# Kernel tuning notes

Measured on AMD Instinct MI355X. Metric: run time of the kernel, lower is better.

The kernel has to match this reference:

```python
import jax, jax.numpy as jnp
import numpy as np

N = 100000      # nodes
E = 1600000     # graph edges
P = 100000      # pos/neg candidate edges
D_IN = 128
D_H = 128
ALPHA = 0.1
NUM_LAYERS = 3


def _linear_params(key, d_in, d_out):
    k1, k2 = jax.random.split(key)
    s = 1.0 / np.sqrt(d_in)
    W = jax.random.uniform(k1, (d_in, d_out), minval=-s, maxval=s, dtype=jnp.float32)
    b = jax.random.uniform(k2, (d_out,), minval=-s, maxval=s, dtype=jnp.float32)
    return W, b


def setup_inputs() -> dict:
    key = jax.random.key(0)
    ks = jax.random.split(key, 12)
    x = jax.random.normal(ks[0], (N, D_IN), dtype=jnp.float32)
    src = jax.random.randint(ks[1], (E,), 0, N)
    dst = jax.random.randint(ks[2], (E,), 0, N)
    pos_src = jax.random.randint(ks[3], (P,), 0, N)
    pos_dst = jax.random.randint(ks[4], (P,), 0, N)
    neg_src = jax.random.randint(ks[5], (P,), 0, N)
    neg_dst = jax.random.randint(ks[6], (P,), 0, N)
    lin1_w, lin1_b = _linear_params(ks[7], D_IN, D_H)
    lin2_w, lin2_b = _linear_params(ks[8], D_H, D_H)
    p1_w, p1_b = _linear_params(ks[9], D_H, D_H)
    p2_w, p2_b = _linear_params(ks[10], D_H, D_H)
    p3_w, p3_b = _linear_params(ks[11], D_H, 1)
    # GPR gamma coefficients: alpha*(1-alpha)^k, last = (1-alpha)^L
    gamma = ALPHA * (1.0 - ALPHA) ** np.arange(NUM_LAYERS + 1, dtype=np.float32)
    gamma[-1] = (1.0 - ALPHA) ** NUM_LAYERS
    gamma = jnp.asarray(gamma, dtype=jnp.float32)
    return {
        "x": x, "lin1_w": lin1_w, "lin1_b": lin1_b, "lin2_w": lin2_w, "lin2_b": lin2_b,
        "gamma": gamma, "p1_w": p1_w, "p1_b": p1_b, "p2_w": p2_w, "p2_b": p2_b,
        "p3_w": p3_w, "p3_b": p3_b,
        "src": src, "dst": dst,
        "pos_src": pos_src, "pos_dst": pos_dst, "neg_src": neg_src, "neg_dst": neg_dst,
    }


def _graph_conv(h, src, dst, n):
    # DGL GraphConv(weight=False, bias=False), norm='both':
    # out = D_in^{-1/2} A (D_out^{-1/2} h), degrees clamped to >= 1
    ones = jnp.ones(src.shape[0], dtype=h.dtype)
    deg_out = jnp.clip(jax.ops.segment_sum(ones, src, num_segments=n), 1.0)
    deg_in = jnp.clip(jax.ops.segment_sum(ones, dst, num_segments=n), 1.0)
    h = h * jax.lax.rsqrt(deg_out)[:, None]
    agg = jax.ops.segment_sum(h[src], dst, num_segments=n)  # [N, D]
    return agg * jax.lax.rsqrt(deg_in)[:, None]


def _predictor(e, p1_w, p1_b, p2_w, p2_b, p3_w, p3_b):
    e = jax.nn.relu(e @ p1_w + p1_b)
    e = jax.nn.relu(e @ p2_w + p2_b)
    return e @ p3_w + p3_b  # [P, 1]


def reference(x, lin1_w, lin1_b, lin2_w, lin2_b, gamma, p1_w, p1_b, p2_w, p2_b,
              p3_w, p3_b, src, dst, pos_src, pos_dst, neg_src, neg_dst):
    n = x.shape[0]
    h = jax.nn.relu(x @ lin1_w + lin1_b)
    h = h @ lin2_w + lin2_b
    rep = gamma[0] * h
    for l in range(NUM_LAYERS):
        h = _graph_conv(h, src, dst, n)
        rep = rep + gamma[l + 1] * h  # full-graph blocks: dstnodes == all nodes
    h = rep
    h_pos = _predictor(h[pos_src] * h[pos_dst], p1_w, p1_b, p2_w, p2_b, p3_w, p3_b)
    h_neg = _predictor(h[neg_src] * h[neg_dst], p1_w, p1_b, p2_w, p2_b, p3_w, p3_b)
    return (h_pos, h_neg)
```

## Files before the change

### kernel.cpp

```cpp
#include <hip/hip_runtime.h>

#define D 128
#define HBINS 16384
#define HCHUNKS 32

typedef _Float16 half8 __attribute__((ext_vector_type(8)));
typedef float floatx4 __attribute__((ext_vector_type(4)));

__host__ __device__ static inline int cdiv(int a, int b){ return (a + b - 1) / b; }

__global__ __launch_bounds__(256) void hist_kernel(const int* __restrict__ vals, int E,
                                                   int* __restrict__ part)
{
    __shared__ int h[HBINS];
    const int r = blockIdx.x / HCHUNKS;
    const int c = blockIdx.x % HCHUNKS;
    for (int i = threadIdx.x; i < HBINS; i += 256) h[i] = 0;
    __syncthreads();

    int elen = cdiv(E, HCHUNKS);
    elen = (elen + 3) & ~3;
    const int lo = c * elen;
    const int hi = min(E, lo + elen);
    if (lo < hi) {
        const int nfull = (hi - lo) >> 2;
        const int4* v4 = (const int4*)(vals + lo);
        for (int i = threadIdx.x; i < nfull; i += 256) {
            const int4 v = v4[i];
            if ((v.x >> 14) == r) atomicAdd(&h[v.x & (HBINS - 1)], 1);
            if ((v.y >> 14) == r) atomicAdd(&h[v.y & (HBINS - 1)], 1);
            if ((v.z >> 14) == r) atomicAdd(&h[v.z & (HBINS - 1)], 1);
            if ((v.w >> 14) == r) atomicAdd(&h[v.w & (HBINS - 1)], 1);
        }
        for (int i = lo + (nfull << 2) + threadIdx.x; i < hi; i += 256) {
            const int v = vals[i];
            if ((v >> 14) == r) atomicAdd(&h[v & (HBINS - 1)], 1);
        }
    }
    __syncthreads();
    int* dstp = part + (size_t)blockIdx.x * HBINS;
    for (int i = threadIdx.x; i < HBINS; i += 256) dstp[i] = h[i];
}

__global__ __launch_bounds__(256) void hist_reduce(const int* __restrict__ partA,
                                                   const int* __restrict__ partB,
                                                   int* __restrict__ cnt_in,
                                                   float* __restrict__ dinv_out,
                                                   float* __restrict__ dinv_in, int n)
{
    const int i = blockIdx.x * 256 + threadIdx.x;
    if (i >= n) return;
    const int r = i >> 14, b = i & (HBINS - 1);
    const size_t base = ((size_t)r * HCHUNKS) * HBINS + b;
    int so = 0, si = 0;
    #pragma unroll
    for (int c = 0; c < HCHUNKS; ++c) {
        so += partA[base + (size_t)c * HBINS];
        si += partB[base + (size_t)c * HBINS];
    }
    dinv_out[i] = rsqrtf(fmaxf((float)so, 1.0f));
    dinv_in[i]  = rsqrtf(fmaxf((float)si, 1.0f));
    cnt_in[i] = si;
}


__global__ __launch_bounds__(256) void scan_partial(const int* __restrict__ cnt,
                                                    int* __restrict__ pre,
                                                    int* __restrict__ blk_sums, int n)
{
    __shared__ int lds[256];
    int t = threadIdx.x;
    int base = blockIdx.x * 1024 + t * 4;
    int v0 = 0, v1 = 0, v2 = 0, v3 = 0;
    if (base + 0 < n) v0 = cnt[base + 0];
    if (base + 1 < n) v1 = cnt[base + 1];
    if (base + 2 < n) v2 = cnt[base + 2];
    if (base + 3 < n) v3 = cnt[base + 3];
    int ts = v0 + v1 + v2 + v3;
    lds[t] = ts;
    __syncthreads();
    for (int off = 1; off < 256; off <<= 1) {
        int add = (t >= off) ? lds[t - off] : 0;
        __syncthreads();
        lds[t] += add;
        __syncthreads();
    }
    int excl = lds[t] - ts;
    if (base + 0 < n) pre[base + 0] = excl;
    if (base + 1 < n) pre[base + 1] = excl + v0;
    if (base + 2 < n) pre[base + 2] = excl + v0 + v1;
    if (base + 3 < n) pre[base + 3] = excl + v0 + v1 + v2;
    if (t == 255) blk_sums[blockIdx.x] = lds[255];
}

__global__ void scan_blk(const int* __restrict__ blk_sums, int* __restrict__ blk_off, int nblk)
{
    if (threadIdx.x == 0 && blockIdx.x == 0) {
        int run = 0;
        for (int j = 0; j < nblk; ++j) { blk_off[j] = run; run += blk_sums[j]; }
    }
}

__global__ __launch_bounds__(256) void scan_final(const int* __restrict__ pre,
                                                  const int* __restrict__ blk_off,
                                                  int* __restrict__ row_start,
                                                  int* __restrict__ fill_ptr, int n, int E)
{
    int i = blockIdx.x * 256 + threadIdx.x;
    if (i < n) {
        int v = pre[i] + blk_off[i >> 10];
        row_start[i] = v;
        fill_ptr[i]  = v;
    }
    if (i == 0) row_start[n] = E;
}

__global__ __launch_bounds__(256) void fill_kernel(const int* __restrict__ src,
                                                   const int* __restrict__ dst,
                                                   int* __restrict__ fill_ptr,
                                                   int* __restrict__ esrc, int E)
{
    int i = blockIdx.x * 256 + threadIdx.x;
    if (i < E) {
        int p = atomicAdd(&fill_ptr[dst[i]], 1);
        esrc[p] = src[i];
    }
}

__global__ __launch_bounds__(256) void wt_kernel(const float* __restrict__ W,
                                                 _Float16* __restrict__ Wt)
{
    __shared__ float tile[32][33];
    const int b = blockIdx.x;
    const int tx = b & 3, ty = b >> 2;
    const int t = threadIdx.x;
    const int r = t >> 3, c4 = (t & 7) * 4;
    const float4 v = *(const float4*)&W[(size_t)(ty * 32 + r) * D + tx * 32 + c4];
    tile[r][c4 + 0] = v.x; tile[r][c4 + 1] = v.y;
    tile[r][c4 + 2] = v.z; tile[r][c4 + 3] = v.w;
    __syncthreads();
    _Float16* dst = Wt + (size_t)(tx * 32 + r) * D + ty * 32 + c4;
    dst[0] = (_Float16)tile[c4 + 0][r];
    dst[1] = (_Float16)tile[c4 + 1][r];
    dst[2] = (_Float16)tile[c4 + 2][r];
    dst[3] = (_Float16)tile[c4 + 3][r];
}

__global__ __launch_bounds__(256, 4) void conv_f16(const _Float16* __restrict__ hin,
                                                   _Float16* __restrict__ hout,
                                                   float* __restrict__ rep,
                                                   const int* __restrict__ row_start,
                                                   const int* __restrict__ esrc,
                                                   const float* __restrict__ dinv_out,
                                                   const float* __restrict__ dinv_in,
                                                   const float* __restrict__ gamma,
                                                   int lidx, int n)
{
    const int node = (blockIdx.x * 256 + threadIdx.x) >> 4;
    const int sub  = threadIdx.x & 15;
    if (node >= n) return;
    const int rs = row_start[node];
    const int re = row_start[node + 1];
    const half8* hb = (const half8*)hin;

    float acc[8] = {0.f, 0.f, 0.f, 0.f, 0.f, 0.f, 0.f, 0.f};
    int i = rs;
    for (; i + 1 < re; i += 2) {
        const int s0 = esrc[i];
        const int s1 = esrc[i + 1];
        const float c0 = dinv_out[s0];
        const float c1 = dinv_out[s1];
        const half8 v0 = hb[(size_t)s0 * 16 + sub];
        const half8 v1 = hb[(size_t)s1 * 16 + sub];
        #pragma unroll
        for (int j = 0; j < 8; ++j)
            acc[j] += (float)v0[j] * c0 + (float)v1[j] * c1;
    }
    if (i < re) {
        const int s0 = esrc[i];
        const float c0 = dinv_out[s0];
        const half8 v0 = hb[(size_t)s0 * 16 + sub];
        #pragma unroll
        for (int j = 0; j < 8; ++j)
            acc[j] += (float)v0[j] * c0;
    }

    const float di = dinv_in[node];
    const float g  = gamma[lidx];
    half8 o;
    #pragma unroll
    for (int j = 0; j < 8; ++j) {
        acc[j] *= di;
        o[j] = (_Float16)acc[j];
    }
    ((half8*)hout)[(size_t)node * 16 + sub] = o;

    floatx4* rp = (floatx4*)(rep + (size_t)node * D + sub * 8);
    floatx4 r0 = rp[0], r1 = rp[1];
    r0[0] += g * acc[0]; r0[1] += g * acc[1]; r0[2] += g * acc[2]; r0[3] += g * acc[3];
    r1[0] += g * acc[4]; r1[1] += g * acc[5]; r1[2] += g * acc[6]; r1[3] += g * acc[7];
    rp[0] = r0; rp[1] = r1;
}

__device__ __forceinline__ int lds_off(int r, int chunk)
{
    return r * D + ((chunk ^ (r & 15)) << 3);
}

template<int MODE>
__global__ __launch_bounds__(256, 2) void gemm_mfma(const float* __restrict__ Xf,
                                                    const _Float16* __restrict__ Xh,
                                                    const _Float16* __restrict__ Wt,
                                                    const float* __restrict__ B, int R,
                                                    _Float16* __restrict__ outh,
                                                    float* __restrict__ rep,
                                                    const float* __restrict__ gamma,
                                                    const int* __restrict__ ia,
                                                    const int* __restrict__ ib,
                                                    const float* __restrict__ w3,
                                                    const float* __restrict__ b3,
                                                    float* __restrict__ outsc)
{
    __shared__ _Float16 Als[D * D];
    __shared__ _Float16 Wls[D * D];
    const int t = threadIdx.x;
    const int rowbase = blockIdx.x * D;

    #pragma unroll
    for (int it = 0; it < 8; ++it) {
        const int r = it * 16 + (t >> 4);
        const int c = t & 15;
        *(half8*)&Wls[lds_off(r, c)] = *(const half8*)(Wt + (size_t)r * D + c * 8);
        int g = rowbase + r; if (g > R - 1) g = R - 1;
        half8 hv;
        if (MODE == 0) {
            const float4* ap = (const float4*)(Xf + (size_t)g * D + c * 8);
            float4 a0 = ap[0], a1 = ap[1];
            hv[0] = (_Float16)a0.x; hv[1] = (_Float16)a0.y;
            hv[2] = (_Float16)a0.z; hv[3] = (_Float16)a0.w;
            hv[4] = (_Float16)a1.x; hv[5] = (_Float16)a1.y;
            hv[6] = (_Float16)a1.z; hv[7] = (_Float16)a1.w;
        } else if (MODE == 2) {
            const float4* pa = (const float4*)(Xf + (size_t)ia[g] * D + c * 8);
            const float4* pb = (const float4*)(Xf + (size_t)ib[g] * D + c * 8);
            float4 a0 = pa[0], a1 = pa[1], b0 = pb[0], b1 = pb[1];
            hv[0] = (_Float16)(a0.x * b0.x); hv[1] = (_Float16)(a0.y * b0.y);
            hv[2] = (_Float16)(a0.z * b0.z); hv[3] = (_Float16)(a0.w * b0.w);
            hv[4] = (_Float16)(a1.x * b1.x); hv[5] = (_Float16)(a1.y * b1.y);
            hv[6] = (_Float16)(a1.z * b1.z); hv[7] = (_Float16)(a1.w * b1.w);
        } else {
            hv = *(const half8*)(Xh + (size_t)g * D + c * 8);
        }
        *(half8*)&Als[lds_off(r, c)] = hv;
    }
    __syncthreads();

    const int wid = t >> 6;
    const int l   = t & 63;
    const int lr  = l & 15;
    const int lq  = l >> 4;

    floatx4 acc[2][8];
    #pragma unroll
    for (int m = 0; m < 2; ++m)
        #pragma unroll
        for (int n = 0; n < 8; ++n) {
            acc[m][n][0] = 0.f; acc[m][n][1] = 0.f;
            acc[m][n][2] = 0.f; acc[m][n][3] = 0.f;
        }

    #pragma unroll
    for (int kk = 0; kk < 4; ++kk) {
        const int cc = kk * 4 + lq;
        half8 af[2], bf[8];
        #pragma unroll
        for (int m = 0; m < 2; ++m) {
            const int r = wid * 32 + m * 16 + lr;
            af[m] = *(half8*)&Als[lds_off(r, cc)];
        }
        #pragma unroll
        for (int n = 0; n < 8; ++n) {
            const int r = n * 16 + lr;
            bf[n] = *(half8*)&Wls[lds_off(r, cc)];
        }
        #pragma unroll
        for (int m = 0; m < 2; ++m)
            #pragma unroll
            for (int n = 0; n < 8; ++n)
                acc[m][n] = __builtin_amdgcn_mfma_f32_16x16x32_f16(af[m], bf[n], acc[m][n], 0, 0, 0);
    }

    if (MODE == 3) {
        float bv[8], wv[8];
        #pragma unroll
        for (int n = 0; n < 8; ++n) { bv[n] = B[n * 16 + lr]; wv[n] = w3[n * 16 + lr]; }
        const float bb = b3[0];
        #pragma unroll
        for (int m = 0; m < 2; ++m) {
            #pragma unroll
            for (int q = 0; q < 4; ++q) {
                float s = 0.f;
                #pragma unroll
                for (int n = 0; n < 8; ++n)
                    s += fmaxf(acc[m][n][q] + bv[n], 0.f) * wv[n];
                s += __shfl_xor(s, 1); s += __shfl_xor(s, 2);
                s += __shfl_xor(s, 4); s += __shfl_xor(s, 8);
                const int r = rowbase + wid * 32 + m * 16 + lq * 4 + q;
                if (lr == 0 && r < R) outsc[r] = s + bb;
            }
        }
    } else {
        float bv[8];
        #pragma unroll
        for (int n = 0; n < 8; ++n) bv[n] = B[n * 16 + lr];
        const float g0 = (MODE == 1) ? gamma[0] : 0.f;
        #pragma unroll
        for (int m = 0; m < 2; ++m) {
            #pragma unroll
            for (int q = 0; q < 4; ++q) {
                const int r = rowbase + wid * 32 + m * 16 + lq * 4 + q;
                if (r < R) {
                    #pragma unroll
                    for (int n = 0; n < 8; ++n) {
                        float v = acc[m][n][q] + bv[n];
                        if (MODE != 1) v = fmaxf(v, 0.f);
                        outh[(size_t)r * D + n * 16 + lr] = (_Float16)v;
                        if (MODE == 1) rep[(size_t)r * D + n * 16 + lr] = g0 * v;
                    }
                }
            }
        }
    }
}


extern "C" void kernel_launch(void* const* d_in, const int* in_sizes, int n_in,
                              void* d_out, int out_size, void* d_ws, size_t ws_size,
                              hipStream_t stream)
{
    const float* x      = (const float*)d_in[0];
    const float* lin1_w = (const float*)d_in[1];
    const float* lin1_b = (const float*)d_in[2];
    const float* lin2_w = (const float*)d_in[3];
    const float* lin2_b = (const float*)d_in[4];
    const float* gamma  = (const float*)d_in[5];
    const float* p1_w   = (const float*)d_in[6];
    const float* p1_b   = (const float*)d_in[7];
    const float* p2_w   = (const float*)d_in[8];
    const float* p2_b   = (const float*)d_in[9];
    const float* p3_w   = (const float*)d_in[10];
    const float* p3_b   = (const float*)d_in[11];
    const int* src     = (const int*)d_in[12];
    const int* dst     = (const int*)d_in[13];
    const int* pos_src = (const int*)d_in[14];
    const int* pos_dst = (const int*)d_in[15];
    const int* neg_src = (const int*)d_in[16];
    const int* neg_dst = (const int*)d_in[17];

    const int N = in_sizes[0] / D;
    const int E = in_sizes[12];
    const int P = in_sizes[14];
    const int NR = cdiv(N, HBINS);

    char* base = (char*)d_ws;
    _Float16* bufB = (_Float16*)base;
    _Float16* bufA = bufB + (size_t)N * D;
    float*    rep  = (float*)(bufA + (size_t)N * D);
    _Float16* wt1  = (_Float16*)(rep + (size_t)N * D);
    _Float16* wt2  = wt1 + D * D;
    _Float16* wtp1 = wt2 + D * D;
    _Float16* wtp2 = wtp1 + D * D;
    char* ip = (char*)(wtp2 + D * D);
    int* cnt_in    = (int*)ip;  ip += (size_t)N * 4;
    int* pre       = (int*)ip;  ip += (size_t)N * 4;
    int* row_start = (int*)ip;  ip += (size_t)(N + 1) * 4;
    int* fill_ptr  = (int*)ip;  ip += (size_t)N * 4;
    int* blk_sums  = (int*)ip;  ip += 4096 * 4;
    int* blk_off   = (int*)ip;  ip += 4096 * 4;
    float* dinv_out = (float*)ip; ip += (size_t)N * 4;
    float* dinv_in  = (float*)ip; ip += (size_t)N * 4;
    int* esrc      = (int*)ip;  ip += (size_t)E * 4;
    int* partA     = (int*)ip;  ip += (size_t)NR * HCHUNKS * HBINS * 4;
    int* partB     = (int*)ip;  ip += (size_t)NR * HCHUNKS * HBINS * 4;
    _Float16* e1;
    if ((size_t)(2 * P) <= 2 * (size_t)N) {
        e1 = (_Float16*)base;
    } else {
        e1 = (_Float16*)ip; ip += (size_t)(2 * P) * D * 2;
    }

    hist_kernel<<<NR * HCHUNKS, 256, 0, stream>>>(src, E, partA);
    hist_kernel<<<NR * HCHUNKS, 256, 0, stream>>>(dst, E, partB);
    hist_reduce<<<cdiv(N, 256), 256, 0, stream>>>(partA, partB, cnt_in,
                                                  dinv_out, dinv_in, N);
    int nblk = cdiv(N, 1024);
    scan_partial<<<nblk, 256, 0, stream>>>(cnt_in, pre, blk_sums, N);
    scan_blk<<<1, 64, 0, stream>>>(blk_sums, blk_off, nblk);
    scan_final<<<cdiv(N, 256), 256, 0, stream>>>(pre, blk_off, row_start, fill_ptr, N, E);
    fill_kernel<<<cdiv(E, 256), 256, 0, stream>>>(src, dst, fill_ptr, esrc, E);

    wt_kernel<<<16, 256, 0, stream>>>(lin1_w, wt1);
    wt_kernel<<<16, 256, 0, stream>>>(lin2_w, wt2);
    wt_kernel<<<16, 256, 0, stream>>>(p1_w, wtp1);
    wt_kernel<<<16, 256, 0, stream>>>(p2_w, wtp2);

    gemm_mfma<0><<<cdiv(N, 128), 256, 0, stream>>>(x, nullptr, wt1, lin1_b, N,
        bufB, nullptr, nullptr, nullptr, nullptr, nullptr, nullptr, nullptr);
    gemm_mfma<1><<<cdiv(N, 128), 256, 0, stream>>>(nullptr, bufB, wt2, lin2_b, N,
        bufA, rep, gamma, nullptr, nullptr, nullptr, nullptr, nullptr);

    conv_f16<<<cdiv(N * 16, 256), 256, 0, stream>>>(bufA, bufB, rep, row_start, esrc,
                                                    dinv_out, dinv_in, gamma, 1, N);
    conv_f16<<<cdiv(N * 16, 256), 256, 0, stream>>>(bufB, bufA, rep, row_start, esrc,
                                                    dinv_out, dinv_in, gamma, 2, N);
    conv_f16<<<cdiv(N * 16, 256), 256, 0, stream>>>(bufA, bufB, rep, row_start, esrc,
                                                    dinv_out, dinv_in, gamma, 3, N);

    gemm_mfma<2><<<cdiv(P, 128), 256, 0, stream>>>(rep, nullptr, wtp1, p1_b, P,
        e1, nullptr, nullptr, pos_src, pos_dst, nullptr, nullptr, nullptr);
    gemm_mfma<2><<<cdiv(P, 128), 256, 0, stream>>>(rep, nullptr, wtp1, p1_b, P,
        e1 + (size_t)P * D, nullptr, nullptr, neg_src, neg_dst, nullptr, nullptr, nullptr);
    gemm_mfma<3><<<cdiv(2 * P, 128), 256, 0, stream>>>(nullptr, e1, wtp2, p2_b, 2 * P,
        nullptr, nullptr, nullptr, nullptr, nullptr, p3_w, p3_b, (float*)d_out);
}
```

Measured before the change: 642.2 us.

## Replace global-atomic CSR fill with per-chunk LDS counting-sort scatter

New measurement: 573.0 us. 1.12x faster.

```diff
diff --git a/kernel.cpp b/kernel.cpp
--- a/kernel.cpp
+++ b/kernel.cpp
@@ -103,27 +103,60 @@
 
 __global__ __launch_bounds__(256) void scan_final(const int* __restrict__ pre,
                                                   const int* __restrict__ blk_off,
-                                                  int* __restrict__ row_start,
-                                                  int* __restrict__ fill_ptr, int n, int E)
+                                                  int* __restrict__ row_start, int n, int E)
 {
     int i = blockIdx.x * 256 + threadIdx.x;
-    if (i < n) {
-        int v = pre[i] + blk_off[i >> 10];
-        row_start[i] = v;
-        fill_ptr[i]  = v;
-    }
+    if (i < n) row_start[i] = pre[i] + blk_off[i >> 10];
     if (i == 0) row_start[n] = E;
 }
 
-__global__ __launch_bounds__(256) void fill_kernel(const int* __restrict__ src,
-                                                   const int* __restrict__ dst,
-                                                   int* __restrict__ fill_ptr,
-                                                   int* __restrict__ esrc, int E)
-{
-    int i = blockIdx.x * 256 + threadIdx.x;
-    if (i < E) {
-        int p = atomicAdd(&fill_ptr[dst[i]], 1);
-        esrc[p] = src[i];
+__global__ __launch_bounds__(256) void cbase_kernel(const int* __restrict__ partB,
+                                                    const int* __restrict__ row_start,
+                                                    int* __restrict__ cb, int n)
+{
+    const int i = blockIdx.x * 256 + threadIdx.x;
+    if (i >= n) return;
+    const int r = i >> 14, b = i & (HBINS - 1);
+    const size_t base = ((size_t)r * HCHUNKS) * HBINS + b;
+    int run = row_start[i];
+    #pragma unroll
+    for (int c = 0; c < HCHUNKS; ++c) {
+        cb[base + (size_t)c * HBINS] = run;
+        run += partB[base + (size_t)c * HBINS];
+    }
+}
+
+__global__ __launch_bounds__(256) void fill_hist(const int* __restrict__ src,
+                                                 const int* __restrict__ dst,
+                                                 const int* __restrict__ cb,
+                                                 int* __restrict__ esrc, int E)
+{
+    __shared__ int h[HBINS];
+    const int r = blockIdx.x / HCHUNKS;
+    const int c = blockIdx.x % HCHUNKS;
+    const int* cbs = cb + (size_t)blockIdx.x * HBINS;
+    for (int i = threadIdx.x; i < HBINS; i += 256) h[i] = cbs[i];
+    __syncthreads();
+
+    int elen = cdiv(E, HCHUNKS);
+    elen = (elen + 3) & ~3;
+    const int lo = c * elen;
+    const int hi = min(E, lo + elen);
+    if (lo >= hi) return;
+    const int nfull = (hi - lo) >> 2;
+    const int4* d4 = (const int4*)(dst + lo);
+    const int4* s4 = (const int4*)(src + lo);
+    for (int i = threadIdx.x; i < nfull; i += 256) {
+        const int4 dv = d4[i];
+        const int4 sv = s4[i];
+        if ((dv.x >> 14) == r) { int p = atomicAdd(&h[dv.x & (HBINS - 1)], 1); esrc[p] = sv.x; }
+        if ((dv.y >> 14) == r) { int p = atomicAdd(&h[dv.y & (HBINS - 1)], 1); esrc[p] = sv.y; }
+        if ((dv.z >> 14) == r) { int p = atomicAdd(&h[dv.z & (HBINS - 1)], 1); esrc[p] = sv.z; }
+        if ((dv.w >> 14) == r) { int p = atomicAdd(&h[dv.w & (HBINS - 1)], 1); esrc[p] = sv.w; }
+    }
+    for (int i = lo + (nfull << 2) + threadIdx.x; i < hi; i += 256) {
+        const int dv = dst[i];
+        if ((dv >> 14) == r) { int p = atomicAdd(&h[dv & (HBINS - 1)], 1); esrc[p] = src[i]; }
     }
 }
 
@@ -374,7 +407,6 @@
     int* cnt_in    = (int*)ip;  ip += (size_t)N * 4;
     int* pre       = (int*)ip;  ip += (size_t)N * 4;
     int* row_start = (int*)ip;  ip += (size_t)(N + 1) * 4;
-    int* fill_ptr  = (int*)ip;  ip += (size_t)N * 4;
     int* blk_sums  = (int*)ip;  ip += 4096 * 4;
     int* blk_off   = (int*)ip;  ip += 4096 * 4;
     float* dinv_out = (float*)ip; ip += (size_t)N * 4;
@@ -382,6 +414,7 @@
     int* esrc      = (int*)ip;  ip += (size_t)E * 4;
     int* partA     = (int*)ip;  ip += (size_t)NR * HCHUNKS * HBINS * 4;
     int* partB     = (int*)ip;  ip += (size_t)NR * HCHUNKS * HBINS * 4;
+    int* cbase     = (int*)ip;  ip += (size_t)NR * HCHUNKS * HBINS * 4;
     _Float16* e1;
     if ((size_t)(2 * P) <= 2 * (size_t)N) {
         e1 = (_Float16*)base;
@@ -396,8 +429,9 @@
     int nblk = cdiv(N, 1024);
     scan_partial<<<nblk, 256, 0, stream>>>(cnt_in, pre, blk_sums, N);
     scan_blk<<<1, 64, 0, stream>>>(blk_sums, blk_off, nblk);
-    scan_final<<<cdiv(N, 256), 256, 0, stream>>>(pre, blk_off, row_start, fill_ptr, N, E);
-    fill_kernel<<<cdiv(E, 256), 256, 0, stream>>>(src, dst, fill_ptr, esrc, E);
+    scan_final<<<cdiv(N, 256), 256, 0, stream>>>(pre, blk_off, row_start, N, E);
+    cbase_kernel<<<cdiv(N, 256), 256, 0, stream>>>(partB, row_start, cbase, N);
+    fill_hist<<<NR * HCHUNKS, 256, 0, stream>>>(src, dst, cbase, esrc, E);
 
     wt_kernel<<<16, 256, 0, stream>>>(lin1_w, wt1);
     wt_kernel<<<16, 256, 0, stream>>>(lin2_w, wt2);
```
